# Optimization experiments

Hardware: AMD Instinct MI355X
Metric: run time of the kernel (lower is better)

Reference implementation:

```python
import jax, jax.numpy as jnp
import numpy as np
import math

G_GRAPHS = 32   # graphs per batch
NPG = 2048      # nodes per graph
DEG = 8         # avg degree
IN_DIM = 128
HID = 128

def _lin(k, fi, fo):
    return jax.random.normal(k, (fi, fo), jnp.float32) / np.sqrt(fi).astype(np.float32)

def setup_inputs():
    key = jax.random.key(0)
    ks = jax.random.split(key, 32)
    Nt = G_GRAPHS * NPG
    Epg = NPG * DEG
    E = G_GRAPHS * Epg
    x = jax.random.normal(ks[0], (Nt, IN_DIM), jnp.float32)
    src = jax.random.randint(ks[1], (E,), 0, NPG)
    dst = jax.random.randint(ks[2], (E,), 0, NPG)
    off = (jnp.arange(E) // Epg) * NPG  # keep edges within their graph block
    edge_index = jnp.stack([src + off, dst + off]).astype(jnp.int32)
    batch = (jnp.arange(Nt) // NPG).astype(jnp.int32)
    p = {}
    dims = [(IN_DIM, HID), (HID, HID), (HID, HID), (HID, HID)]
    for i, (fi, fo) in enumerate(dims, 1):
        p['Wl%d' % i] = _lin(ks[3 * i], fi, fo)
        p['bl%d' % i] = jnp.zeros((fo,), jnp.float32)
        p['Wr%d' % i] = _lin(ks[3 * i + 1], fi, fo)
    for j in (1, 2):  # SAGPooling score GNN (GraphConv hidden->1)
        p['Prel%d' % j] = _lin(ks[15 + 2 * j], HID, 1)
        p['prb%d' % j] = jnp.zeros((1,), jnp.float32)
        p['Proot%d' % j] = _lin(ks[16 + 2 * j], HID, 1)
    p['W5'] = _lin(ks[24], HID, 64); p['b5'] = jnp.zeros((64,), jnp.float32)
    p['W6'] = _lin(ks[25], 64, 2);  p['b6'] = jnp.zeros((2,), jnp.float32)
    return dict(x=x, edge_index=edge_index, batch=batch, npg=NPG, **p)

def reference(x, edge_index, batch, npg,
              Wl1, bl1, Wr1, Wl2, bl2, Wr2, Wl3, bl3, Wr3, Wl4, bl4, Wr4,
              Prel1, prb1, Proot1, Prel2, prb2, Proot2, W5, b5, W6, b6):
    src, dst = edge_index[0], edge_index[1]
    Nt = x.shape[0]
    Gn = Nt // npg

    def sage(h, em, Wl, bl, Wr):
        # SAGEConv (mean aggr): lin_l(mean_j x_j) + lin_r(x_root)
        s = jax.ops.segment_sum(h[src] * em[:, None], dst, num_segments=Nt)
        c = jax.ops.segment_sum(em, dst, num_segments=Nt)
        return (s / jnp.maximum(c, 1.0)[:, None]) @ Wl + bl + h @ Wr

    def pool(h, em, nm, k, Prel, prb, Proot):
        # SAGPooling: score = GraphConv(h) (add aggr), top-k per graph, x *= tanh(score)
        s = jax.ops.segment_sum(h[src] * em[:, None], dst, num_segments=Nt)
        score = (s @ Prel + h @ Proot + prb)[:, 0]
        smr = jnp.where(nm > 0, score, -1e30).reshape(Gn, npg)
        _, idx = jax.lax.top_k(smr, k)
        newm = jnp.zeros((Gn, npg), h.dtype).at[jnp.arange(Gn)[:, None], idx].set(1.0).reshape(-1)
        h = h * jnp.tanh(score)[:, None] * newm[:, None]
        em = em * newm[src] * newm[dst]  # filter_adj: keep edges with both ends kept
        return h, em, newm

    em = jnp.ones(src.shape, x.dtype)
    nm = jnp.ones((Nt,), x.dtype)
    h = jax.nn.relu(sage(x, em, Wl1, bl1, Wr1))
    h = jax.nn.relu(sage(h, em, Wl2, bl2, Wr2))
    k1 = math.ceil(0.5 * npg)
    h, em, nm = pool(h, em, nm, k1, Prel1, prb1, Proot1)
    h = jax.nn.relu(sage(h, em, Wl3, bl3, Wr3)) * nm[:, None]
    h = jax.nn.relu(sage(h, em, Wl4, bl4, Wr4)) * nm[:, None]
    k2 = math.ceil(0.5 * k1)
    h, em, nm = pool(h, em, nm, k2, Prel2, prb2, Proot2)
    # global mean pool over surviving nodes
    sums = jax.ops.segment_sum(h, batch, num_segments=Gn)
    cnt = jax.ops.segment_sum(nm, batch, num_segments=Gn)
    g = sums / jnp.maximum(cnt, 1.0)[:, None]
    g = jax.nn.relu(g @ W5 + b5)
    return jax.nn.log_softmax(g @ W6 + b6, axis=1)
```

## Files before the change

kernel.cpp:

```cpp
#include <hip/hip_runtime.h>
#include <hip/hip_bf16.h>
#include <math.h>

#define NT   65536
#define NPGC 2048
#define NG   32
#define NE   524288
#define HID  128

typedef short short8 __attribute__((ext_vector_type(8)));
typedef float f32x4  __attribute__((ext_vector_type(4)));

__device__ __forceinline__ float bf2f(unsigned short u) {
    union { unsigned int i; float f; } v; v.i = ((unsigned int)u) << 16; return v.f;
}
__device__ __forceinline__ unsigned short f2bf(float f) {
    union { float f; unsigned int i; } v; v.f = f;
    unsigned int x = v.i;
    return (unsigned short)((x + 0x7fffu + ((x >> 16) & 1u)) >> 16);
}

__global__ void k_detect(const unsigned short* __restrict__ x, int* __restrict__ flag) {
    __shared__ int cnt;
    if (threadIdx.x == 0) cnt = 0;
    __syncthreads();
    int sane = 0;
#pragma unroll
    for (int j = 0; j < 16; ++j) {
        unsigned short u = x[threadIdx.x * 16 + j];
        int e = (u >> 7) & 0xFF;
        if (e > 0x60 && e < 0xA0) sane++;
    }
    atomicAdd(&cnt, sane);
    __syncthreads();
    if (threadIdx.x == 0) *flag = (cnt > 3686) ? 1 : 0;
}

struct CvtDesc { const void* src[22]; int n[22]; int off[22]; };

__global__ void k_cvt(CvtDesc d, float* __restrict__ wts, const int* __restrict__ flag) {
    int t = blockIdx.y;
    int n = d.n[t];
    bool isbf = (*flag != 0);
    const unsigned short* sb = (const unsigned short*)d.src[t];
    const float* sf = (const float*)d.src[t];
    float* o = wts + d.off[t];
    for (int i = blockIdx.x * blockDim.x + threadIdx.x; i < n; i += gridDim.x * blockDim.x)
        o[i] = isbf ? bf2f(sb[i]) : sf[i];
}

__global__ void k_packW(const float* __restrict__ wts, int4 oWl, int4 oWr,
                        unsigned short* __restrict__ Wpack) {
    int idx = blockIdx.x * 256 + threadIdx.x;
    if (idx >= 4 * 8 * 8 * 64 * 8) return;
    int L    = idx >> 15;
    int rem  = idx & 32767;
    int ct   = rem >> 12;
    int rem2 = rem & 4095;
    int ks   = rem2 >> 9;
    int rem3 = rem2 & 511;
    int lane = rem3 >> 3;
    int j    = rem3 & 7;
    int k   = ks * 32 + (lane >> 4) * 8 + j;
    int col = ct * 16 + (lane & 15);
    int ol = (L == 0) ? oWl.x : (L == 1) ? oWl.y : (L == 2) ? oWl.z : oWl.w;
    int orr = (L == 0) ? oWr.x : (L == 1) ? oWr.y : (L == 2) ? oWr.z : oWr.w;
    float w = (k < 128) ? wts[ol + k * 128 + col] : wts[orr + (k - 128) * 128 + col];
    unsigned short hi = f2bf(w);
    unsigned short lo = f2bf(w - bf2f(hi));
    int base = L * 65536 + (ct * 8 + ks) * 512 + lane * 8 + j;
    Wpack[base]         = hi;
    Wpack[base + 32768] = lo;
}

__global__ void k_load_x(const void* __restrict__ x, float* __restrict__ out,
                         const int* __restrict__ flag, int n4,
                         float* __restrict__ nm, int* __restrict__ rowc, int* __restrict__ fill) {
    int i = blockIdx.x * blockDim.x + threadIdx.x;
    if (i < NT) { nm[i] = 1.0f; rowc[i] = 0; fill[i] = 0; }
    if (i >= n4) return;
    if (*flag) {
        ushort4 v = ((const ushort4*)x)[i];
        float4 o;
        o.x = bf2f(v.x); o.y = bf2f(v.y); o.z = bf2f(v.z); o.w = bf2f(v.w);
        ((float4*)out)[i] = o;
    } else {
        ((float4*)out)[i] = ((const float4*)x)[i];
    }
}

__global__ void k_hist(const int* __restrict__ dst, int* __restrict__ cnt) {
    int e = blockIdx.x * blockDim.x + threadIdx.x;
    if (e < NE) atomicAdd(&cnt[dst[e]], 1);
}

__global__ void k_scan1(const int* __restrict__ cnt, int* __restrict__ rp, int* __restrict__ bsum,
                        float* __restrict__ invc) {
    __shared__ int s[256];
    int t = threadIdx.x;
    int i = blockIdx.x * 256 + t;
    int v = cnt[i];
    invc[i] = 1.0f / fmaxf((float)v, 1.0f);
    s[t] = v;
    __syncthreads();
    for (int off = 1; off < 256; off <<= 1) {
        int a = (t >= off) ? s[t - off] : 0;
        __syncthreads();
        s[t] += a;
        __syncthreads();
    }
    rp[i] = s[t] - v;
    if (t == 255) bsum[blockIdx.x] = s[255];
}

__global__ void k_scan2(const int* __restrict__ bsum, int* __restrict__ boff) {
    __shared__ int s[256];
    int t = threadIdx.x;
    int v = bsum[t];
    s[t] = v;
    __syncthreads();
    for (int off = 1; off < 256; off <<= 1) {
        int a = (t >= off) ? s[t - off] : 0;
        __syncthreads();
        s[t] += a;
        __syncthreads();
    }
    boff[t] = s[t] - v;
}

__global__ void k_scan3(int* __restrict__ rp, const int* __restrict__ boff) {
    int i = blockIdx.x * 256 + threadIdx.x;
    rp[i] += boff[i >> 8];
    if (i == 0) rp[NT] = NE;
}

__global__ void k_scatter(const int* __restrict__ src, const int* __restrict__ dst,
                          const int* __restrict__ rp, int* __restrict__ fill, int* __restrict__ col) {
    int e = blockIdx.x * blockDim.x + threadIdx.x;
    if (e < NE) {
        int d = dst[e];
        int p = rp[d] + atomicAdd(&fill[d], 1);
        col[p] = src[e];
    }
}

__device__ __forceinline__ int lds_sw(int node, int k) {
    int g = k >> 3;
    int go = g ^ (node & 7);
    return node * 128 + go * 8 + (k & 7);
}

template<bool HAS_TS>
__device__ __forceinline__ void sage_body(
    const float* __restrict__ h, const float* __restrict__ ts,
    const float* __restrict__ invc,
    const int* __restrict__ rp, const int* __restrict__ col,
    const unsigned short* __restrict__ Wp,
    unsigned short* Ahi, unsigned short* Alo,
    int n0, int tid, f32x4 acc[2][2])
{
    int lane = tid & 63, w = tid >> 6;
    int lrow = lane & 15, quad = lane >> 4;

#pragma unroll
    for (int pass = 0; pass < 4; ++pass) {
        int node = pass * 8 + (tid >> 5);
        int f = (tid & 31) * 4;
        int gn = n0 + node;
        int beg = rp[gn], end = rp[gn + 1];
        float ax = 0.f, ay = 0.f, az = 0.f, aw = 0.f;
        for (int e0 = beg; e0 < end; e0 += 4) {
            int ecl = end - 1;
            int e1 = (e0 + 1 < end) ? e0 + 1 : ecl;
            int e2 = (e0 + 2 < end) ? e0 + 2 : ecl;
            int e3 = (e0 + 3 < end) ? e0 + 3 : ecl;
            int s0 = col[e0], s1 = col[e1], s2 = col[e2], s3 = col[e3];
            float4 v0 = *(const float4*)&h[(size_t)s0 * HID + f];
            float4 v1 = *(const float4*)&h[(size_t)s1 * HID + f];
            float4 v2 = *(const float4*)&h[(size_t)s2 * HID + f];
            float4 v3 = *(const float4*)&h[(size_t)s3 * HID + f];
            float c0 = HAS_TS ? ts[s0] : 1.0f;
            float c1 = (e0 + 1 < end) ? (HAS_TS ? ts[s1] : 1.0f) : 0.0f;
            float c2 = (e0 + 2 < end) ? (HAS_TS ? ts[s2] : 1.0f) : 0.0f;
            float c3 = (e0 + 3 < end) ? (HAS_TS ? ts[s3] : 1.0f) : 0.0f;
            ax += v0.x * c0 + v1.x * c1 + v2.x * c2 + v3.x * c3;
            ay += v0.y * c0 + v1.y * c1 + v2.y * c2 + v3.y * c3;
            az += v0.z * c0 + v1.z * c1 + v2.z * c2 + v3.z * c3;
            aw += v0.w * c0 + v1.w * c1 + v2.w * c2 + v3.w * c3;
        }
        float inv = invc[gn];
        float m0 = ax * inv, m1 = ay * inv, m2 = az * inv, m3 = aw * inv;
        ushort4 hi4, lo4;
        hi4.x = f2bf(m0); lo4.x = f2bf(m0 - bf2f(hi4.x));
        hi4.y = f2bf(m1); lo4.y = f2bf(m1 - bf2f(hi4.y));
        hi4.z = f2bf(m2); lo4.z = f2bf(m2 - bf2f(hi4.z));
        hi4.w = f2bf(m3); lo4.w = f2bf(m3 - bf2f(hi4.w));
        int a = lds_sw(node, f);
        *(ushort4*)&Ahi[a] = hi4;
        *(ushort4*)&Alo[a] = lo4;
    }
    __syncthreads();

#pragma unroll
    for (int ks = 0; ks < 4; ++ks) {
        short8 bh[2], blo[2];
#pragma unroll
        for (int c = 0; c < 2; ++c) {
            int ct = 2 * w + c;
            bh[c]  = *(const short8*)&Wp[(ct * 8 + ks) * 512 + lane * 8];
            blo[c] = *(const short8*)&Wp[32768 + (ct * 8 + ks) * 512 + lane * 8];
        }
        int kb = ks * 32 + quad * 8;
#pragma unroll
        for (int st = 0; st < 2; ++st) {
            int a = lds_sw(st * 16 + lrow, kb);
            short8 ah = *(const short8*)&Ahi[a];
            short8 al = *(const short8*)&Alo[a];
#pragma unroll
            for (int c = 0; c < 2; ++c) {
                acc[st][c] = __builtin_amdgcn_mfma_f32_16x16x32_bf16(ah, bh[c],  acc[st][c], 0, 0, 0);
                acc[st][c] = __builtin_amdgcn_mfma_f32_16x16x32_bf16(al, bh[c],  acc[st][c], 0, 0, 0);
                acc[st][c] = __builtin_amdgcn_mfma_f32_16x16x32_bf16(ah, blo[c], acc[st][c], 0, 0, 0);
            }
        }
    }
    __syncthreads();

#pragma unroll
    for (int i = 0; i < 4; ++i) {
        int idx = i * 256 + tid;
        int node = idx >> 5;
        int f = (idx & 31) * 4;
        int gn = n0 + node;
        float4 v = *(const float4*)&h[(size_t)gn * HID + f];
        float sc = HAS_TS ? ts[gn] : 1.0f;
        float v0 = v.x * sc, v1 = v.y * sc, v2 = v.z * sc, v3 = v.w * sc;
        ushort4 hi4, lo4;
        hi4.x = f2bf(v0); lo4.x = f2bf(v0 - bf2f(hi4.x));
        hi4.y = f2bf(v1); lo4.y = f2bf(v1 - bf2f(hi4.y));
        hi4.z = f2bf(v2); lo4.z = f2bf(v2 - bf2f(hi4.z));
        hi4.w = f2bf(v3); lo4.w = f2bf(v3 - bf2f(hi4.w));
        int a = lds_sw(node, f);
        *(ushort4*)&Ahi[a] = hi4;
        *(ushort4*)&Alo[a] = lo4;
    }
    __syncthreads();

#pragma unroll
    for (int ks = 4; ks < 8; ++ks) {
        short8 bh[2], blo[2];
#pragma unroll
        for (int c = 0; c < 2; ++c) {
            int ct = 2 * w + c;
            bh[c]  = *(const short8*)&Wp[(ct * 8 + ks) * 512 + lane * 8];
            blo[c] = *(const short8*)&Wp[32768 + (ct * 8 + ks) * 512 + lane * 8];
        }
        int kb = (ks - 4) * 32 + quad * 8;
#pragma unroll
        for (int st = 0; st < 2; ++st) {
            int a = lds_sw(st * 16 + lrow, kb);
            short8 ah = *(const short8*)&Ahi[a];
            short8 al = *(const short8*)&Alo[a];
#pragma unroll
            for (int c = 0; c < 2; ++c) {
                acc[st][c] = __builtin_amdgcn_mfma_f32_16x16x32_bf16(ah, bh[c],  acc[st][c], 0, 0, 0);
                acc[st][c] = __builtin_amdgcn_mfma_f32_16x16x32_bf16(al, bh[c],  acc[st][c], 0, 0, 0);
                acc[st][c] = __builtin_amdgcn_mfma_f32_16x16x32_bf16(ah, blo[c], acc[st][c], 0, 0, 0);
            }
        }
    }
}

template<bool HAS_TS>
__global__ void __launch_bounds__(256, 8) k_sage_plain(
    const float* __restrict__ h, const float* __restrict__ ts,
    const float* __restrict__ nm, const float* __restrict__ invc,
    const int* __restrict__ rp, const int* __restrict__ col,
    const unsigned short* __restrict__ Wp, const float* __restrict__ bl,
    float* __restrict__ out)
{
    __shared__ unsigned short Ahi[32 * 128];
    __shared__ unsigned short Alo[32 * 128];
    int tid = threadIdx.x;
    int b = blockIdx.x;
    int graph = (b & 7) * 4 + (b >> 9);
    int tile  = (b >> 3) & 63;
    int n0 = graph * NPGC + tile * 32;
    int lane = tid & 63, w = tid >> 6;
    int lrow = lane & 15, quad = lane >> 4;
    f32x4 acc[2][2] = {};

    sage_body<HAS_TS>(h, ts, invc, rp, col, Wp, Ahi, Alo, n0, tid, acc);

#pragma unroll
    for (int c = 0; c < 2; ++c) {
        int colg = (2 * w + c) * 16 + lrow;
        float bias = bl[colg];
#pragma unroll
        for (int st = 0; st < 2; ++st) {
#pragma unroll
            for (int rr = 0; rr < 4; ++rr) {
                int node = n0 + st * 16 + quad * 4 + rr;
                float val = fmaxf(acc[st][c][rr] + bias, 0.f) * nm[node];
                out[(size_t)node * HID + colg] = val;
            }
        }
    }
}

__global__ void __launch_bounds__(256, 8) k_sage_dots(
    const float* __restrict__ h,
    const float* __restrict__ nm, const float* __restrict__ invc,
    const int* __restrict__ rp, const int* __restrict__ col,
    const unsigned short* __restrict__ Wp, const float* __restrict__ bl,
    float* __restrict__ out,
    const float* __restrict__ Prel, const float* __restrict__ Proot,
    float* __restrict__ q, float* __restrict__ r)
{
    __shared__ unsigned short Ahi[32 * 128];
    __shared__ unsigned short Alo[32 * 128];
    int tid = threadIdx.x;
    int b = blockIdx.x;
    int graph = (b & 7) * 4 + (b >> 9);
    int tile  = (b >> 3) & 63;
    int n0 = graph * NPGC + tile * 32;
    int lane = tid & 63, w = tid >> 6;
    int lrow = lane & 15, quad = lane >> 4;
    f32x4 acc[2][2] = {};

    sage_body<false>(h, nullptr, invc, rp, col, Wp, Ahi, Alo, n0, tid, acc);

    float qp[2][4] = {}, rp_[2][4] = {};
#pragma unroll
    for (int c = 0; c < 2; ++c) {
        int colg = (2 * w + c) * 16 + lrow;
        float bias = bl[colg];
        float pq = Prel[colg], pr = Proot[colg];
#pragma unroll
        for (int st = 0; st < 2; ++st) {
#pragma unroll
            for (int rr = 0; rr < 4; ++rr) {
                int node = n0 + st * 16 + quad * 4 + rr;
                float val = fmaxf(acc[st][c][rr] + bias, 0.f) * nm[node];
                out[(size_t)node * HID + colg] = val;
                qp[st][rr] += val * pq;
                rp_[st][rr] += val * pr;
            }
        }
    }
#pragma unroll
    for (int st = 0; st < 2; ++st)
#pragma unroll
        for (int rr = 0; rr < 4; ++rr) {
#pragma unroll
            for (int m = 1; m < 16; m <<= 1) {
                qp[st][rr]  += __shfl_xor(qp[st][rr],  m, 64);
                rp_[st][rr] += __shfl_xor(rp_[st][rr], m, 64);
            }
        }
    __syncthreads();
    float* qa = (float*)Ahi;
    if (tid < 64) qa[tid] = 0.f;
    __syncthreads();
    if (lrow == 0) {
#pragma unroll
        for (int st = 0; st < 2; ++st)
#pragma unroll
            for (int rr = 0; rr < 4; ++rr) {
                int nl = st * 16 + quad * 4 + rr;
                atomicAdd(&qa[nl], qp[st][rr]);
                atomicAdd(&qa[32 + nl], rp_[st][rr]);
            }
    }
    __syncthreads();
    if (tid < 32) {
        q[n0 + tid] = qa[tid];
        r[n0 + tid] = qa[32 + tid];
    }
}

__global__ void k_score(const float* __restrict__ q, const float* __restrict__ r,
                        const float* __restrict__ prb,
                        const int* __restrict__ rp, const int* __restrict__ col,
                        float* __restrict__ score) {
    int n = blockIdx.x * 256 + threadIdx.x;
    int beg = rp[n], end = rp[n + 1];
    float s = 0.f;
    for (int e = beg; e < end; ++e) s += q[col[e]];
    score[n] = s + r[n] + prb[0];
}

__global__ void __launch_bounds__(256) k_topk(const float* __restrict__ score,
                                              float* __restrict__ nm,
                                              float* __restrict__ tval, int k,
                                              const int* __restrict__ rp,
                                              const int* __restrict__ col,
                                              float* __restrict__ invc, int doInvc) {
    __shared__ unsigned int u[NPGC];
    __shared__ unsigned char msk[NPGC];
    __shared__ int hist[256];
    __shared__ int scanb[256];
    __shared__ unsigned int s_byte;
    __shared__ int s_kk;
    int tid = threadIdx.x;
    int base = blockIdx.x * NPGC;

    for (int j = tid; j < NPGC; j += 256) {
        float sc = (nm[base + j] > 0.f) ? score[base + j] : -1e30f;
        unsigned int v = __float_as_uint(sc);
        v = (v & 0x80000000u) ? ~v : (v | 0x80000000u);
        u[j] = v;
    }
    __syncthreads();

    unsigned int prefix = 0;
    int kk = k;
#pragma unroll
    for (int round = 0; round < 4; ++round) {
        int shift = 24 - 8 * round;
        unsigned int pmask = (round == 0) ? 0u : (0xFFFFFFFFu << (32 - 8 * round));
        hist[tid] = 0;
        __syncthreads();
        for (int j = tid; j < NPGC; j += 256) {
            unsigned int v = u[j];
            if ((v & pmask) == prefix) atomicAdd(&hist[(v >> shift) & 0xFF], 1);
        }
        __syncthreads();
        scanb[tid] = hist[tid];
        __syncthreads();
        for (int off = 1; off < 256; off <<= 1) {
            int add = (tid + off < 256) ? scanb[tid + off] : 0;
            __syncthreads();
            scanb[tid] += add;
            __syncthreads();
        }
        int above = (tid == 255) ? 0 : scanb[tid + 1];
        if (scanb[tid] >= kk && above < kk) {
            s_byte = (unsigned int)tid;
            s_kk = kk - above;
        }
        __syncthreads();
        prefix |= (s_byte << shift);
        kk = s_kk;
        __syncthreads();
    }
    unsigned int thr = prefix;
    int j0 = tid * 8;
    int cnt = 0;
#pragma unroll
    for (int j = 0; j < 8; ++j) cnt += (u[j0 + j] == thr);
    scanb[tid] = cnt;
    __syncthreads();
    for (int off = 1; off < 256; off <<= 1) {
        int add = (tid >= off) ? scanb[tid - off] : 0;
        __syncthreads();
        scanb[tid] += add;
        __syncthreads();
    }
    int rank = scanb[tid] - cnt;
#pragma unroll
    for (int j = 0; j < 8; ++j) {
        unsigned int v = u[j0 + j];
        bool keep;
        if (v > thr) keep = true;
        else if (v == thr) { keep = (rank < kk); rank++; }
        else keep = false;
        msk[j0 + j] = keep ? 1 : 0;
        nm[base + j0 + j]   = keep ? 1.0f : 0.0f;
        tval[base + j0 + j] = keep ? tanhf(score[base + j0 + j]) : 0.0f;
    }

    if (doInvc) {
        __syncthreads();
        for (int n = tid; n < NPGC; n += 256) {
            int gn = base + n;
            int beg = rp[gn], end = rp[gn + 1];
            float c = 0.f;
            for (int e = beg; e < end; ++e) c += (float)msk[col[e] - base];
            invc[gn] = 1.0f / fmaxf(c, 1.0f);
        }
    }
}

__global__ void k_gsum(const float* __restrict__ h, const float* __restrict__ t,
                       const float* __restrict__ nm,
                       float* __restrict__ g, float* __restrict__ gcnt) {
    int b = blockIdx.x;
    int graph = b >> 4, part = b & 15;
    int f = threadIdx.x & 127, sub = threadIdx.x >> 7;
    int nbase = graph * NPGC + part * 128 + sub * 64;
    float acc = 0.f;
#pragma unroll 4
    for (int n = 0; n < 64; ++n)
        acc += h[(size_t)(nbase + n) * HID + f] * t[nbase + n];
    atomicAdd(&g[graph * HID + f], acc);
    if (threadIdx.x < 64 && sub == 0) {
        float cnt = 0.f;
        int cb = graph * NPGC + part * 128;
        for (int n = threadIdx.x; n < 128; n += 64) cnt += nm[cb + n];
        for (int o = 32; o > 0; o >>= 1) cnt += __shfl_down(cnt, o, 64);
        if (threadIdx.x == 0) atomicAdd(&gcnt[graph], cnt);
    }
}

__global__ void k_gdiv(float* __restrict__ g, const float* __restrict__ gcnt) {
    int i = blockIdx.x * 256 + threadIdx.x;
    if (i < NG * HID) g[i] /= fmaxf(gcnt[i >> 7], 1.0f);
}

__global__ void k_mlp(const float* __restrict__ g, const float* __restrict__ W5,
                      const float* __restrict__ b5, const float* __restrict__ W6,
                      const float* __restrict__ b6, void* __restrict__ out,
                      const int* __restrict__ flag) {
    __shared__ float g5[64];
    __shared__ float ls[2];
    int graph = blockIdx.x, j = threadIdx.x;
    float acc = b5[j];
    for (int f = 0; f < HID; ++f)
        acc += g[graph * HID + f] * W5[f * 64 + j];
    g5[j] = fmaxf(acc, 0.f);
    __syncthreads();
    if (j < 2) {
        float l = b6[j];
        for (int t = 0; t < 64; ++t) l += g5[t] * W6[t * 2 + j];
        ls[j] = l;
    }
    __syncthreads();
    if (j == 0) {
        float a = ls[0], b = ls[1];
        float mx = fmaxf(a, b);
        float lse = mx + logf(expf(a - mx) + expf(b - mx));
        if (*flag) {
            ((unsigned short*)out)[graph * 2 + 0] = f2bf(a - lse);
            ((unsigned short*)out)[graph * 2 + 1] = f2bf(b - lse);
        } else {
            ((float*)out)[graph * 2 + 0] = a - lse;
            ((float*)out)[graph * 2 + 1] = b - lse;
        }
    }
}

extern "C" void kernel_launch(void* const* d_in, const int* in_sizes, int n_in,
                              void* d_out, int out_size, void* d_ws, size_t ws_size,
                              hipStream_t stream) {
    const void* x    = d_in[0];
    const int*  ei   = (const int*)d_in[1];
    const int*  srcE = ei;
    const int*  dstE = ei + NE;

    char* ws = (char*)d_ws;
    float* hA    = (float*)(ws + 0);
    float* hB    = (float*)(ws + 33554432);
    float* tvec  = (float*)(ws + 67108864);
    float* invc  = (float*)(ws + 67371008);
    float* q     = (float*)(ws + 100663296);
    float* r     = (float*)(ws + 100925440);
    float* score = (float*)(ws + 101187584);
    float* nm    = (float*)(ws + 101449728);
    int*   rowc  = (int*)  (ws + 101711872);
    int*   rp    = (int*)  (ws + 101974016);
    int*   bsum  = (int*)  (ws + 102236416);
    int*   boff  = (int*)  (ws + 102237440);
    int*   fill  = (int*)  (ws + 102238464);
    int*   col   = (int*)  (ws + 102500608);
    float* g     = (float*)(ws + 104597760);
    float* gcnt  = (float*)(ws + 104614144);
    int*   flag  = (int*)  (ws + 104615936);
    float* wts   = (float*)(ws + 104616960);
    unsigned short* Wpack = (unsigned short*)(ws + 105179136);
    (void)in_sizes; (void)n_in; (void)out_size; (void)ws_size;

    const int O_Wl1 = 0,      O_bl1 = 16384,  O_Wr1 = 16512;
    const int O_Wl2 = 32896,  O_bl2 = 49280,  O_Wr2 = 49408;
    const int O_Wl3 = 65792,  O_bl3 = 82176,  O_Wr3 = 82304;
    const int O_Wl4 = 98688,  O_bl4 = 115072, O_Wr4 = 115200;
    const int O_Pr1 = 131584, O_pb1 = 131712, O_Po1 = 131713;
    const int O_Pr2 = 131841, O_pb2 = 131969, O_Po2 = 131970;
    const int O_W5  = 132098, O_b5  = 140290, O_W6 = 140354, O_b6 = 140482;

    CvtDesc d;
    const int srcIdx[22] = {4,5,6,7,8,9,10,11,12,13,14,15,16,17,18,19,20,21,22,23,24,25};
    const int nelems[22] = {16384,128,16384, 16384,128,16384, 16384,128,16384, 16384,128,16384,
                            128,1,128, 128,1,128, 8192,64,128,2};
    const int offs[22]   = {O_Wl1,O_bl1,O_Wr1, O_Wl2,O_bl2,O_Wr2, O_Wl3,O_bl3,O_Wr3, O_Wl4,O_bl4,O_Wr4,
                            O_Pr1,O_pb1,O_Po1, O_Pr2,O_pb2,O_Po2, O_W5,O_b5,O_W6,O_b6};
    for (int i = 0; i < 22; ++i) { d.src[i] = d_in[srcIdx[i]]; d.n[i] = nelems[i]; d.off[i] = offs[i]; }

    hipMemsetAsync(g, 0, (NG * HID + NG + 64) * 4, stream);

    k_detect <<<1, 256, 0, stream>>>((const unsigned short*)x, flag);
    k_cvt    <<<dim3(64, 22), 256, 0, stream>>>(d, wts, flag);
    k_packW  <<<512, 256, 0, stream>>>(wts, make_int4(O_Wl1, O_Wl2, O_Wl3, O_Wl4),
                                       make_int4(O_Wr1, O_Wr2, O_Wr3, O_Wr4), Wpack);
    k_load_x <<<8192, 256, 0, stream>>>(x, hA, flag, NT * HID / 4, nm, rowc, fill);

    k_hist   <<<2048, 256, 0, stream>>>(dstE, rowc);
    k_scan1  <<<256, 256, 0, stream>>>(rowc, rp, bsum, invc);
    k_scan2  <<<1, 256, 0, stream>>>(bsum, boff);
    k_scan3  <<<256, 256, 0, stream>>>(rp, boff);
    k_scatter<<<2048, 256, 0, stream>>>(srcE, dstE, rp, fill, col);

    k_sage_plain<false><<<2048, 256, 0, stream>>>(hA, nullptr, nm, invc, rp, col,
                                                  Wpack + 0 * 65536, wts + O_bl1, hB);
    k_sage_dots<<<2048, 256, 0, stream>>>(hB, nm, invc, rp, col,
                                          Wpack + 1 * 65536, wts + O_bl2, hA,
                                          wts + O_Pr1, wts + O_Po1, q, r);

    k_score<<<256, 256, 0, stream>>>(q, r, wts + O_pb1, rp, col, score);
    k_topk <<<32, 256, 0, stream>>>(score, nm, tvec, 1024, rp, col, invc, 1);

    k_sage_plain<true><<<2048, 256, 0, stream>>>(hA, tvec, nm, invc, rp, col,
                                                 Wpack + 2 * 65536, wts + O_bl3, hB);
    k_sage_dots<<<2048, 256, 0, stream>>>(hB, nm, invc, rp, col,
                                          Wpack + 3 * 65536, wts + O_bl4, hA,
                                          wts + O_Pr2, wts + O_Po2, q, r);

    k_score<<<256, 256, 0, stream>>>(q, r, wts + O_pb2, rp, col, score);
    k_topk <<<32, 256, 0, stream>>>(score, nm, tvec, 512, rp, col, invc, 0);

    k_gsum<<<512, 256, 0, stream>>>(hA, tvec, nm, g, gcnt);
    k_gdiv<<<16, 256, 0, stream>>>(g, gcnt);
    k_mlp <<<32, 64, 0, stream>>>(g, wts + O_W5, wts + O_b5, wts + O_W6, wts + O_b6, d_out, flag);
}
```

Measured before the change: 417.2 us.

## Fuse small kernels and skip aggregation for pooled-out nodes

Merges the histogram into the x-load kernel (moving counter zeroing to the weight-pack kernel), folds the score gather into top-k, and folds the mean division into the MLP. This removes four launches and an intermediate score buffer. It also skips neighbor aggregation for nodes whose mask is zero, cutting gather traffic after pooling. The tradeoff is that the score gather now runs in only 32 blocks, one per graph, which lowers parallelism for that step.

```diff
diff --git a/kernel.cpp b/kernel.cpp
--- a/kernel.cpp
+++ b/kernel.cpp
@@ -50,8 +50,10 @@
 }
 
 __global__ void k_packW(const float* __restrict__ wts, int4 oWl, int4 oWr,
-                        unsigned short* __restrict__ Wpack) {
+                        unsigned short* __restrict__ Wpack,
+                        int* __restrict__ rowc, int* __restrict__ fill) {
     int idx = blockIdx.x * 256 + threadIdx.x;
+    if (idx < NT) { rowc[idx] = 0; fill[idx] = 0; }
     if (idx >= 4 * 8 * 8 * 64 * 8) return;
     int L    = idx >> 15;
     int rem  = idx & 32767;
@@ -75,9 +77,11 @@
 
 __global__ void k_load_x(const void* __restrict__ x, float* __restrict__ out,
                          const int* __restrict__ flag, int n4,
-                         float* __restrict__ nm, int* __restrict__ rowc, int* __restrict__ fill) {
+                         float* __restrict__ nm, const int* __restrict__ dstE,
+                         int* __restrict__ rowc) {
     int i = blockIdx.x * blockDim.x + threadIdx.x;
-    if (i < NT) { nm[i] = 1.0f; rowc[i] = 0; fill[i] = 0; }
+    if (i < NT) nm[i] = 1.0f;
+    if (i < NE) atomicAdd(&rowc[dstE[i]], 1);
     if (i >= n4) return;
     if (*flag) {
         ushort4 v = ((const ushort4*)x)[i];
@@ -89,11 +93,6 @@
     }
 }
 
-__global__ void k_hist(const int* __restrict__ dst, int* __restrict__ cnt) {
-    int e = blockIdx.x * blockDim.x + threadIdx.x;
-    if (e < NE) atomicAdd(&cnt[dst[e]], 1);
-}
-
 __global__ void k_scan1(const int* __restrict__ cnt, int* __restrict__ rp, int* __restrict__ bsum,
                         float* __restrict__ invc) {
     __shared__ int s[256];
@@ -153,7 +152,7 @@
 template<bool HAS_TS>
 __device__ __forceinline__ void sage_body(
     const float* __restrict__ h, const float* __restrict__ ts,
-    const float* __restrict__ invc,
+    const float* __restrict__ nm, const float* __restrict__ invc,
     const int* __restrict__ rp, const int* __restrict__ col,
     const unsigned short* __restrict__ Wp,
     unsigned short* Ahi, unsigned short* Alo,
@@ -167,26 +166,28 @@
         int node = pass * 8 + (tid >> 5);
         int f = (tid & 31) * 4;
         int gn = n0 + node;
-        int beg = rp[gn], end = rp[gn + 1];
         float ax = 0.f, ay = 0.f, az = 0.f, aw = 0.f;
-        for (int e0 = beg; e0 < end; e0 += 4) {
-            int ecl = end - 1;
-            int e1 = (e0 + 1 < end) ? e0 + 1 : ecl;
-            int e2 = (e0 + 2 < end) ? e0 + 2 : ecl;
-            int e3 = (e0 + 3 < end) ? e0 + 3 : ecl;
-            int s0 = col[e0], s1 = col[e1], s2 = col[e2], s3 = col[e3];
-            float4 v0 = *(const float4*)&h[(size_t)s0 * HID + f];
-            float4 v1 = *(const float4*)&h[(size_t)s1 * HID + f];
-            float4 v2 = *(const float4*)&h[(size_t)s2 * HID + f];
-            float4 v3 = *(const float4*)&h[(size_t)s3 * HID + f];
-            float c0 = HAS_TS ? ts[s0] : 1.0f;
-            float c1 = (e0 + 1 < end) ? (HAS_TS ? ts[s1] : 1.0f) : 0.0f;
-            float c2 = (e0 + 2 < end) ? (HAS_TS ? ts[s2] : 1.0f) : 0.0f;
-            float c3 = (e0 + 3 < end) ? (HAS_TS ? ts[s3] : 1.0f) : 0.0f;
-            ax += v0.x * c0 + v1.x * c1 + v2.x * c2 + v3.x * c3;
-            ay += v0.y * c0 + v1.y * c1 + v2.y * c2 + v3.y * c3;
-            az += v0.z * c0 + v1.z * c1 + v2.z * c2 + v3.z * c3;
-            aw += v0.w * c0 + v1.w * c1 + v2.w * c2 + v3.w * c3;
+        if (nm[gn] > 0.f) {
+            int beg = rp[gn], end = rp[gn + 1];
+            for (int e0 = beg; e0 < end; e0 += 4) {
+                int ecl = end - 1;
+                int e1 = (e0 + 1 < end) ? e0 + 1 : ecl;
+                int e2 = (e0 + 2 < end) ? e0 + 2 : ecl;
+                int e3 = (e0 + 3 < end) ? e0 + 3 : ecl;
+                int s0 = col[e0], s1 = col[e1], s2 = col[e2], s3 = col[e3];
+                float4 v0 = *(const float4*)&h[(size_t)s0 * HID + f];
+                float4 v1 = *(const float4*)&h[(size_t)s1 * HID + f];
+                float4 v2 = *(const float4*)&h[(size_t)s2 * HID + f];
+                float4 v3 = *(const float4*)&h[(size_t)s3 * HID + f];
+                float c0 = HAS_TS ? ts[s0] : 1.0f;
+                float c1 = (e0 + 1 < end) ? (HAS_TS ? ts[s1] : 1.0f) : 0.0f;
+                float c2 = (e0 + 2 < end) ? (HAS_TS ? ts[s2] : 1.0f) : 0.0f;
+                float c3 = (e0 + 3 < end) ? (HAS_TS ? ts[s3] : 1.0f) : 0.0f;
+                ax += v0.x * c0 + v1.x * c1 + v2.x * c2 + v3.x * c3;
+                ay += v0.y * c0 + v1.y * c1 + v2.y * c2 + v3.y * c3;
+                az += v0.z * c0 + v1.z * c1 + v2.z * c2 + v3.z * c3;
+                aw += v0.w * c0 + v1.w * c1 + v2.w * c2 + v3.w * c3;
+            }
         }
         float inv = invc[gn];
         float m0 = ax * inv, m1 = ay * inv, m2 = az * inv, m3 = aw * inv;
@@ -290,7 +291,7 @@
     int lrow = lane & 15, quad = lane >> 4;
     f32x4 acc[2][2] = {};
 
-    sage_body<HAS_TS>(h, ts, invc, rp, col, Wp, Ahi, Alo, n0, tid, acc);
+    sage_body<HAS_TS>(h, ts, nm, invc, rp, col, Wp, Ahi, Alo, n0, tid, acc);
 
 #pragma unroll
     for (int c = 0; c < 2; ++c) {
@@ -328,7 +329,7 @@
     int lrow = lane & 15, quad = lane >> 4;
     f32x4 acc[2][2] = {};
 
-    sage_body<false>(h, nullptr, invc, rp, col, Wp, Ahi, Alo, n0, tid, acc);
+    sage_body<false>(h, nullptr, nm, invc, rp, col, Wp, Ahi, Alo, n0, tid, acc);
 
     float qp[2][4] = {}, rp_[2][4] = {};
 #pragma unroll
@@ -379,24 +380,16 @@
     }
 }
 
-__global__ void k_score(const float* __restrict__ q, const float* __restrict__ r,
-                        const float* __restrict__ prb,
-                        const int* __restrict__ rp, const int* __restrict__ col,
-                        float* __restrict__ score) {
-    int n = blockIdx.x * 256 + threadIdx.x;
-    int beg = rp[n], end = rp[n + 1];
-    float s = 0.f;
-    for (int e = beg; e < end; ++e) s += q[col[e]];
-    score[n] = s + r[n] + prb[0];
-}
-
-__global__ void __launch_bounds__(256) k_topk(const float* __restrict__ score,
+__global__ void __launch_bounds__(256) k_topk(const float* __restrict__ q,
+                                              const float* __restrict__ rv,
+                                              const float* __restrict__ prb,
                                               float* __restrict__ nm,
                                               float* __restrict__ tval, int k,
                                               const int* __restrict__ rp,
                                               const int* __restrict__ col,
                                               float* __restrict__ invc, int doInvc) {
     __shared__ unsigned int u[NPGC];
+    __shared__ float scl[NPGC];
     __shared__ unsigned char msk[NPGC];
     __shared__ int hist[256];
     __shared__ int scanb[256];
@@ -404,10 +397,17 @@
     __shared__ int s_kk;
     int tid = threadIdx.x;
     int base = blockIdx.x * NPGC;
+    float pb = prb[0];
 
     for (int j = tid; j < NPGC; j += 256) {
-        float sc = (nm[base + j] > 0.f) ? score[base + j] : -1e30f;
-        unsigned int v = __float_as_uint(sc);
+        int gn = base + j;
+        int beg = rp[gn], end = rp[gn + 1];
+        float s = 0.f;
+        for (int e = beg; e < end; ++e) s += q[col[e]];
+        float sc = s + rv[gn] + pb;
+        scl[j] = sc;
+        float scm = (nm[gn] > 0.f) ? sc : -1e30f;
+        unsigned int v = __float_as_uint(scm);
         v = (v & 0x80000000u) ? ~v : (v | 0x80000000u);
         u[j] = v;
     }
@@ -467,7 +467,7 @@
         else keep = false;
         msk[j0 + j] = keep ? 1 : 0;
         nm[base + j0 + j]   = keep ? 1.0f : 0.0f;
-        tval[base + j0 + j] = keep ? tanhf(score[base + j0 + j]) : 0.0f;
+        tval[base + j0 + j] = keep ? tanhf(scl[j0 + j]) : 0.0f;
     }
 
     if (doInvc) {
@@ -503,21 +503,18 @@
     }
 }
 
-__global__ void k_gdiv(float* __restrict__ g, const float* __restrict__ gcnt) {
-    int i = blockIdx.x * 256 + threadIdx.x;
-    if (i < NG * HID) g[i] /= fmaxf(gcnt[i >> 7], 1.0f);
-}
-
-__global__ void k_mlp(const float* __restrict__ g, const float* __restrict__ W5,
+__global__ void k_mlp(const float* __restrict__ g, const float* __restrict__ gcnt,
+                      const float* __restrict__ W5,
                       const float* __restrict__ b5, const float* __restrict__ W6,
                       const float* __restrict__ b6, void* __restrict__ out,
                       const int* __restrict__ flag) {
     __shared__ float g5[64];
     __shared__ float ls[2];
     int graph = blockIdx.x, j = threadIdx.x;
+    float ic = 1.0f / fmaxf(gcnt[graph], 1.0f);
     float acc = b5[j];
     for (int f = 0; f < HID; ++f)
-        acc += g[graph * HID + f] * W5[f * 64 + j];
+        acc += (g[graph * HID + f] * ic) * W5[f * 64 + j];
     g5[j] = fmaxf(acc, 0.f);
     __syncthreads();
     if (j < 2) {
@@ -555,7 +552,6 @@
     float* invc  = (float*)(ws + 67371008);
     float* q     = (float*)(ws + 100663296);
     float* r     = (float*)(ws + 100925440);
-    float* score = (float*)(ws + 101187584);
     float* nm    = (float*)(ws + 101449728);
     int*   rowc  = (int*)  (ws + 101711872);
     int*   rp    = (int*)  (ws + 101974016);
@@ -591,10 +587,9 @@
     k_detect <<<1, 256, 0, stream>>>((const unsigned short*)x, flag);
     k_cvt    <<<dim3(64, 22), 256, 0, stream>>>(d, wts, flag);
     k_packW  <<<512, 256, 0, stream>>>(wts, make_int4(O_Wl1, O_Wl2, O_Wl3, O_Wl4),
-                                       make_int4(O_Wr1, O_Wr2, O_Wr3, O_Wr4), Wpack);
-    k_load_x <<<8192, 256, 0, stream>>>(x, hA, flag, NT * HID / 4, nm, rowc, fill);
-
-    k_hist   <<<2048, 256, 0, stream>>>(dstE, rowc);
+                                       make_int4(O_Wr1, O_Wr2, O_Wr3, O_Wr4), Wpack, rowc, fill);
+    k_load_x <<<8192, 256, 0, stream>>>(x, hA, flag, NT * HID / 4, nm, dstE, rowc);
+
     k_scan1  <<<256, 256, 0, stream>>>(rowc, rp, bsum, invc);
     k_scan2  <<<1, 256, 0, stream>>>(bsum, boff);
     k_scan3  <<<256, 256, 0, stream>>>(rp, boff);
@@ -606,8 +601,7 @@
                                           Wpack + 1 * 65536, wts + O_bl2, hA,
                                           wts + O_Pr1, wts + O_Po1, q, r);
 
-    k_score<<<256, 256, 0, stream>>>(q, r, wts + O_pb1, rp, col, score);
-    k_topk <<<32, 256, 0, stream>>>(score, nm, tvec, 1024, rp, col, invc, 1);
+    k_topk<<<32, 256, 0, stream>>>(q, r, wts + O_pb1, nm, tvec, 1024, rp, col, invc, 1);
 
     k_sage_plain<true><<<2048, 256, 0, stream>>>(hA, tvec, nm, invc, rp, col,
                                                  Wpack + 2 * 65536, wts + O_bl3, hB);
@@ -615,10 +609,8 @@
                                           Wpack + 3 * 65536, wts + O_bl4, hA,
                                           wts + O_Pr2, wts + O_Po2, q, r);
 
-    k_score<<<256, 256, 0, stream>>>(q, r, wts + O_pb2, rp, col, score);
-    k_topk <<<32, 256, 0, stream>>>(score, nm, tvec, 512, rp, col, invc, 0);
+    k_topk<<<32, 256, 0, stream>>>(q, r, wts + O_pb2, nm, tvec, 512, rp, col, invc, 0);
 
     k_gsum<<<512, 256, 0, stream>>>(hA, tvec, nm, g, gcnt);
-    k_gdiv<<<16, 256, 0, stream>>>(g, gcnt);
-    k_mlp <<<32, 64, 0, stream>>>(g, wts + O_W5, wts + O_b5, wts + O_W6, wts + O_b6, d_out, flag);
-}
+    k_mlp <<<32, 64, 0, stream>>>(g, gcnt, wts + O_W5, wts + O_b5, wts + O_W6, wts + O_b6, d_out, flag);
+}
```

Result: slower. 446.5 us (+7.0%).
